# Kernel optimization log

Measured on AMD Instinct MI355X. Metric: run time of the kernel, lower is better.

## Reference

```python
import jax, jax.numpy as jnp
import numpy as np
import math

D_MODEL, N_HEADS, BATCH, SEQ = 1024, 16, 2, 2048
D_HEAD = D_MODEL // N_HEADS


def setup_inputs() -> dict:
    key = jax.random.key(0)
    ks = jax.random.split(key, 5)
    w = lambda k: jax.random.normal(k, (D_MODEL, D_MODEL), jnp.float32) * 0.02
    return {
        "X": jax.random.normal(ks[0], (BATCH, SEQ, D_MODEL), jnp.float32),
        "W_q": w(ks[1]),
        "W_k": w(ks[2]),
        "W_v": w(ks[3]),
        "W_o": w(ks[4]),
        "g_q": jnp.ones((D_MODEL,), jnp.float32),
        "b_q": jnp.zeros((D_MODEL,), jnp.float32),
        "g_k": jnp.ones((D_MODEL,), jnp.float32),
        "b_k": jnp.zeros((D_MODEL,), jnp.float32),
        "cache_k": jnp.zeros((BATCH, N_HEADS, SEQ, D_HEAD), jnp.float32),
        "cache_v": jnp.zeros((BATCH, N_HEADS, SEQ, D_HEAD), jnp.float32),
        "start_pos": 0,
    }


def _layernorm(x, g, b, eps=1e-5):
    mu = jnp.mean(x, axis=-1, keepdims=True)
    xc = x - mu
    var = jnp.mean(xc * xc, axis=-1, keepdims=True)
    return xc * jax.lax.rsqrt(var + eps) * g + b


def reference(X, W_q, W_k, W_v, W_o, g_q, b_q, g_k, b_k, cache_k, cache_v, start_pos):
    batch, N, d_model = X.shape
    H = cache_k.shape[1]
    dh = d_model // H

    # QK-normed projections (torch Linear: x @ W^T)
    XQ = _layernorm(X @ W_q.T, g_q, b_q)
    XK = _layernorm(X @ W_k.T, g_k, b_k)
    XV = X @ W_v.T
    split = lambda t: t.reshape(batch, N, H, dh).transpose(0, 2, 1, 3)  # [b,h,n,d]
    XQ, XK, XV = split(XQ), split(XK), split(XV)

    # KV-cache scatter update, then slice to valid prefix (start_pos is static)
    cache_k = jax.lax.dynamic_update_slice(cache_k, XK, (0, 0, start_pos, 0))
    cache_v = jax.lax.dynamic_update_slice(cache_v, XV, (0, 0, start_pos, 0))
    M = start_pos + N
    K = cache_k[:, :, :M]
    V = cache_v[:, :, :M]

    logits = jnp.einsum('bhnd,bhmd->bhnm', XQ, K) / math.sqrt(dh)  # [b,h,N,M]

    # causal mask on the freshly written block [start_pos:M]
    tril = jnp.tril(jnp.ones((N, N), bool))
    full_mask = jnp.concatenate([jnp.ones((N, start_pos), bool), tril], axis=1)  # [N,M]
    logits = jnp.where(full_mask[None, None], logits, -jnp.inf)

    # selective forget-mask bias built from relu'd head-0 logits
    S = jax.nn.relu(logits[:, 0])               # relu(-inf) -> 0, matches torch
    S = S.at[..., 0].set(0.0)                   # zero first column
    S = S * (1.0 - jnp.eye(N, dtype=S.dtype))   # zero diagonal (valid since start_pos==0)
    S = jnp.roll(S, 1, axis=-2)                 # shift rows down by one
    S = S.at[..., 0, :].set(0.0)
    F_mask = jnp.cumsum(S, axis=-2)             # [b,N,M]

    logits = logits - F_mask[:, None]
    attn = jax.nn.softmax(logits, axis=-1)
    O = jnp.einsum('bhnm,bhmd->bhnd', attn, V)
    O = O.transpose(0, 2, 1, 3).reshape(batch, N, d_model)
    return O @ W_o.T
```

## Files before the change

### kernel.cpp

```cpp
#include <hip/hip_runtime.h>
#include <cstdint>
#include <cstddef>


typedef unsigned short u16;
typedef __attribute__((ext_vector_type(8))) __bf16 bf16x8;
typedef __attribute__((ext_vector_type(4))) float f32x4;
typedef __attribute__((ext_vector_type(2))) unsigned int uint2v;

#define D_MODEL 1024
#define N_HEADS 16
#define BATCH   2
#define SEQ     2048
#define D_HEAD  64
#define ROWS    (BATCH*SEQ)
#define NSEG    64
#define SEGLEN  32
#define LOG2E   1.44269504f

static __device__ __forceinline__ u16 f2bf(float f){
  union { float f; uint32_t u; } v; v.f = f;
  uint32_t r = v.u + 0x7fffu + ((v.u >> 16) & 1u);
  return (u16)(r >> 16);
}
static __device__ __forceinline__ float bf2f(u16 h){
  union { uint32_t u; float f; } v; v.u = ((uint32_t)h) << 16;
  return v.f;
}
static __device__ __forceinline__ uint32_t cvtpk(float lo, float hi){
  uint32_t r;
  asm("v_cvt_pk_bf16_f32 %0, %1, %2" : "=v"(r) : "v"(lo), "v"(hi));
  return r;
}
#define GLDS(gp, lp) __builtin_amdgcn_global_load_lds( \
    (const __attribute__((address_space(1))) void*)(gp), \
    (__attribute__((address_space(3))) void*)(lp), 16, 0, 0)

__global__ void k_cast_all(const float* __restrict__ X,
                           u16* __restrict__ Xhi, u16* __restrict__ Xlo,
                           const float* __restrict__ Wq,
                           u16* __restrict__ Wqh, u16* __restrict__ Wql,
                           const float* __restrict__ Wk,
                           u16* __restrict__ Wkh, u16* __restrict__ Wkl,
                           const float* __restrict__ Wv, u16* __restrict__ Wvb,
                           const float* __restrict__ Wo, u16* __restrict__ Wob){
  int i = blockIdx.x*256 + threadIdx.x;
  if (i < 1572864){
    const float* src; u16 *dh, *dl; int base;
    if (i < 1048576){ src = X;  dh = Xhi; dl = Xlo; base = i; }
    else if (i < 1310720){ src = Wq; dh = Wqh; dl = Wql; base = i - 1048576; }
    else { src = Wk; dh = Wkh; dl = Wkl; base = i - 1310720; }
    float4 v = reinterpret_cast<const float4*>(src)[base];
    float vs[4] = {v.x, v.y, v.z, v.w};
    union { u16 s[4]; uint2 u; } uh, ul;
#pragma unroll
    for (int r=0;r<4;++r){
      uh.s[r] = f2bf(vs[r]);
      ul.s[r] = f2bf(vs[r] - bf2f(uh.s[r]));
    }
    reinterpret_cast<uint2*>(dh)[base] = uh.u;
    reinterpret_cast<uint2*>(dl)[base] = ul.u;
  } else {
    const float* src; u16* dst; int base;
    if (i < 1835008){ src = Wv; dst = Wvb; base = i - 1572864; }
    else { src = Wo; dst = Wob; base = i - 1835008; }
    float4 v = reinterpret_cast<const float4*>(src)[base];
    float vs[4] = {v.x, v.y, v.z, v.w};
    union { u16 s[4]; uint2 u; } uh;
#pragma unroll
    for (int r=0;r<4;++r) uh.s[r] = f2bf(vs[r]);
    reinterpret_cast<uint2*>(dst)[base] = uh.u;
  }
}

__global__ __launch_bounds__(256) void k_mega(
    const u16* __restrict__ Xhi, const u16* __restrict__ Xlo,
    const u16* __restrict__ Wh,  const u16* __restrict__ Wl,
    const u16* __restrict__ Wvb,
    float* __restrict__ C, float* __restrict__ Dlt, u16* __restrict__ Vt)
{
  __shared__ __align__(16) u16 smem[16384];
  const int xj = blockIdx.x & 7, q = blockIdx.x >> 3;
  int section, idx;
  if (q < 64)      { section = 0; idx = xj*64 + q; }
  else if (q < 128){ section = 1; idx = xj*64 + (q-64); }
  else             { section = 2; idx = xj*16 + (q-128); }
  const int tid = threadIdx.x, wv = tid>>6, ln = tid&63;
  const int lane15 = ln&15, quad = ln>>4;
  const int wm = wv&1, wn = wv>>1;
  const int g = ln&7, sr = ln>>3;
  const int fs = lane15 & 7;
  f32x4 z = {0.f,0.f,0.f,0.f};
  u16* As = smem;
  u16* Bs = smem + 8192;

  if (section == 2){
    const int cx = idx & 1;
    const int cy = (idx >> 1) & 31;
    const int cz = idx >> 6;
    const size_t rowBase = (size_t)cy*128;
    const size_t wbase = cx ? (size_t)1024*1024 : 0;
    const u16* Ap = cz ? Xlo : Xhi;
    const u16* Bp = (cz ? Wh : Wl) + wbase;
    f32x4 acc[4][2];
#pragma unroll
    for (int i=0;i<4;++i){ acc[i][0] = z; acc[i][1] = z; }
    for (int kt = 0; kt < 16; ++kt) {
      __syncthreads();
#pragma unroll
      for (int c = 0; c < 4; ++c) {
        int chunk = wv*4 + c, r = chunk*8 + sr;
        GLDS(Ap + (rowBase + r)*1024 + kt*64 + (g^sr)*8, As + chunk*512);
      }
#pragma unroll
      for (int c = 0; c < 2; ++c) {
        int chunk = wv*2 + c, r = chunk*8 + sr;
        GLDS(Bp + (size_t)r*1024 + kt*64 + (g^sr)*8, Bs + chunk*512);
      }
      __syncthreads();
#pragma unroll
      for (int k2=0;k2<2;++k2){
        bf16x8 af[4], bfb[2];
#pragma unroll
        for (int t=0;t<4;++t)
          af[t]  = *reinterpret_cast<const bf16x8*>(As + (wm*64 + t*16 + lane15)*64 + (((k2*4+quad)^fs)*8));
#pragma unroll
        for (int t=0;t<2;++t)
          bfb[t] = *reinterpret_cast<const bf16x8*>(Bs + (wn*32 + t*16 + lane15)*64 + (((k2*4+quad)^fs)*8));
#pragma unroll
        for (int i=0;i<4;++i)
#pragma unroll
          for (int j=0;j<2;++j)
            acc[i][j] = __builtin_amdgcn_mfma_f32_16x16x32_bf16(af[i], bfb[j], acc[i][j], 0,0,0);
      }
    }
    float* Dp = Dlt + (size_t)cz*ROWS*128;
#pragma unroll
    for (int i=0;i<4;++i){
      size_t row = rowBase + wm*64 + i*16 + quad*4;
#pragma unroll
      for (int j=0;j<2;++j){
        size_t col = (size_t)cx*64 + wn*32 + j*16 + lane15;
#pragma unroll
        for (int r=0;r<4;++r)
          Dp[(row+r)*128 + col] = acc[i][j][r];
      }
    }
  } else if (section == 0){
    const size_t rowBase = (size_t)(idx>>4)*128, colBase = (size_t)(idx&15)*128;
    f32x4 acc[4][4];
#pragma unroll
    for (int i=0;i<4;++i)
#pragma unroll
      for (int j=0;j<4;++j) acc[i][j] = z;
    for (int kt = 0; kt < 16; ++kt) {
      __syncthreads();
#pragma unroll
      for (int c = 0; c < 4; ++c) {
        int chunk = wv*4 + c, r = chunk*8 + sr;
        GLDS(Xhi + (rowBase + r)*1024 + kt*64 + (g^sr)*8, As + chunk*512);
        GLDS(Wh  + (colBase + r)*1024 + kt*64 + (g^sr)*8, Bs + chunk*512);
      }
      __syncthreads();
#pragma unroll
      for (int k2=0;k2<2;++k2){
        bf16x8 af[4], bfb[4];
#pragma unroll
        for (int t=0;t<4;++t){
          af[t]  = *reinterpret_cast<const bf16x8*>(As + (wm*64 + t*16 + lane15)*64 + (((k2*4+quad)^fs)*8));
          bfb[t] = *reinterpret_cast<const bf16x8*>(Bs + (wn*64 + t*16 + lane15)*64 + (((k2*4+quad)^fs)*8));
        }
#pragma unroll
        for (int i=0;i<4;++i)
#pragma unroll
          for (int j=0;j<4;++j)
            acc[i][j] = __builtin_amdgcn_mfma_f32_16x16x32_bf16(af[i], bfb[j], acc[i][j], 0,0,0);
      }
    }
#pragma unroll
    for (int i=0;i<4;++i){
      size_t row = rowBase + wm*64 + i*16 + quad*4;
#pragma unroll
      for (int j=0;j<4;++j){
        size_t col = colBase + wn*64 + j*16 + lane15;
#pragma unroll
        for (int r=0;r<4;++r)
          C[(row+r)*2048 + col] = acc[i][j][r];
      }
    }
  } else {
    const int bx = idx & 15, by = idx >> 4;
    const size_t rowBase = (size_t)by*128, colBase = (size_t)bx*64;
    f32x4 acc[4][2];
#pragma unroll
    for (int i=0;i<4;++i){ acc[i][0] = z; acc[i][1] = z; }
    for (int kt = 0; kt < 16; ++kt) {
      __syncthreads();
#pragma unroll
      for (int c = 0; c < 4; ++c) {
        int chunk = wv*4 + c, r = chunk*8 + sr;
        GLDS(Xhi + (rowBase + r)*1024 + kt*64 + (g^sr)*8, As + chunk*512);
      }
#pragma unroll
      for (int c = 0; c < 2; ++c) {
        int chunk = wv*2 + c, r = chunk*8 + sr;
        GLDS(Wvb + (colBase + r)*1024 + kt*64 + (g^sr)*8, Bs + chunk*512);
      }
      __syncthreads();
#pragma unroll
      for (int k2=0;k2<2;++k2){
        bf16x8 af[4], bfb[2];
#pragma unroll
        for (int t=0;t<4;++t)
          af[t]  = *reinterpret_cast<const bf16x8*>(As + (wm*64 + t*16 + lane15)*64 + (((k2*4+quad)^fs)*8));
#pragma unroll
        for (int t=0;t<2;++t)
          bfb[t] = *reinterpret_cast<const bf16x8*>(Bs + (wn*32 + t*16 + lane15)*64 + (((k2*4+quad)^fs)*8));
#pragma unroll
        for (int i=0;i<4;++i)
#pragma unroll
          for (int j=0;j<2;++j)
            acc[i][j] = __builtin_amdgcn_mfma_f32_16x16x32_bf16(af[i], bfb[j], acc[i][j], 0,0,0);
      }
    }
    __syncthreads();
#pragma unroll
    for (int i=0;i<4;++i){
      int nl = wm*64 + i*16 + quad*4;
#pragma unroll
      for (int j=0;j<2;++j){
        int dl = wn*32 + j*16 + lane15;
#pragma unroll
        for (int r=0;r<4;++r)
          smem[dl*136 + nl + r] = f2bf(acc[i][j][r]);
      }
    }
    __syncthreads();
    const int b = by >> 4;
    const int n0 = (by & 15) * 128;
    const int bh = b*N_HEADS + bx;
    const int d = tid >> 2, seg = tid & 3;
    u16* dst = Vt + ((size_t)(bh*64 + d))*SEQ + n0 + seg*32;
    const u16* srcl = smem + d*136 + seg*32;
#pragma unroll
    for (int k=0;k<4;++k)
      *reinterpret_cast<uint4*>(dst + k*8) = *reinterpret_cast<const uint4*>(srcl + k*8);
  }
}

__global__ __launch_bounds__(256) void k_ln_pack2(
    const float* __restrict__ C, const float* __restrict__ Dlt,
    const float* __restrict__ gq, const float* __restrict__ bq,
    const float* __restrict__ gk, const float* __restrict__ bk,
    u16* __restrict__ Qh, u16* __restrict__ Kh,
    u16* __restrict__ Q0l, u16* __restrict__ K0l)
{
  const int row = blockIdx.x;
  const int tid = threadIdx.x;
  const float* cr = C + (size_t)row*2048;
  float4 vq = reinterpret_cast<const float4*>(cr)[tid];
  float4 vk = reinterpret_cast<const float4*>(cr)[256 + tid];
  const int h = tid >> 4;
  if (h == 0){
    const float* D0 = Dlt + (size_t)row*128;
    const float* D1 = Dlt + (size_t)ROWS*128 + (size_t)row*128;
    float4 a0 = reinterpret_cast<const float4*>(D0)[tid&15];
    float4 a1 = reinterpret_cast<const float4*>(D1)[tid&15];
    vq.x+=a0.x+a1.x; vq.y+=a0.y+a1.y; vq.z+=a0.z+a1.z; vq.w+=a0.w+a1.w;
    float4 b0 = reinterpret_cast<const float4*>(D0 + 64)[tid&15];
    float4 b1 = reinterpret_cast<const float4*>(D1 + 64)[tid&15];
    vk.x+=b0.x+b1.x; vk.y+=b0.y+b1.y; vk.z+=b0.z+b1.z; vk.w+=b0.w+b1.w;
  }
  float sq  = vq.x+vq.y+vq.z+vq.w;
  float s2q = vq.x*vq.x+vq.y*vq.y+vq.z*vq.z+vq.w*vq.w;
  float sk  = vk.x+vk.y+vk.z+vk.w;
  float s2k = vk.x*vk.x+vk.y*vk.y+vk.z*vk.z+vk.w*vk.w;
#pragma unroll
  for (int o=32;o;o>>=1){
    sq += __shfl_xor(sq,o);  s2q += __shfl_xor(s2q,o);
    sk += __shfl_xor(sk,o);  s2k += __shfl_xor(s2k,o);
  }
  __shared__ float red[4][4];
  if ((tid&63)==0){
    red[tid>>6][0]=sq; red[tid>>6][1]=s2q; red[tid>>6][2]=sk; red[tid>>6][3]=s2k;
  }
  __syncthreads();
  sq  = red[0][0]+red[1][0]+red[2][0]+red[3][0];
  s2q = red[0][1]+red[1][1]+red[2][1]+red[3][1];
  sk  = red[0][2]+red[1][2]+red[2][2]+red[3][2];
  s2k = red[0][3]+red[1][3]+red[2][3]+red[3][3];
  const float muq = sq*(1.f/D_MODEL);
  const float rsq = rsqrtf(s2q*(1.f/D_MODEL) - muq*muq + 1e-5f);
  const float muk = sk*(1.f/D_MODEL);
  const float rsk = rsqrtf(s2k*(1.f/D_MODEL) - muk*muk + 1e-5f);
  const int b = row >> 11, n = row & (SEQ-1);
  const int d0 = (tid & 15)*4;
  float4 gqv = reinterpret_cast<const float4*>(gq)[tid];
  float4 bqv = reinterpret_cast<const float4*>(bq)[tid];
  float4 gkv = reinterpret_cast<const float4*>(gk)[tid];
  float4 bkv = reinterpret_cast<const float4*>(bk)[tid];
  float xq[4] = {vq.x,vq.y,vq.z,vq.w}, xk[4] = {vk.x,vk.y,vk.z,vk.w};
  float gQ[4] = {gqv.x,gqv.y,gqv.z,gqv.w}, bQ[4] = {bqv.x,bqv.y,bqv.z,bqv.w};
  float gK[4] = {gkv.x,gkv.y,gkv.z,gkv.w}, bK[4] = {bkv.x,bkv.y,bkv.z,bkv.w};
  union { u16 s[4]; uint2 u; } qh, ql, kh, kl;
#pragma unroll
  for (int r=0;r<4;++r){
    float yq = (xq[r]-muq)*rsq*gQ[r] + bQ[r];
    qh.s[r] = f2bf(yq);
    ql.s[r] = f2bf(yq - bf2f(qh.s[r]));
    float yk = (xk[r]-muk)*rsk*gK[r] + bK[r];
    kh.s[r] = f2bf(yk);
    kl.s[r] = f2bf(yk - bf2f(kh.s[r]));
  }
  size_t dst = (((size_t)(b*N_HEADS + h))*SEQ + n)*D_HEAD + d0;
  *reinterpret_cast<uint2*>(Qh + dst) = qh.u;
  *reinterpret_cast<uint2*>(Kh + dst) = kh.u;
  if (h == 0){
    size_t dl = ((size_t)b*SEQ + n)*D_HEAD + d0;
    *reinterpret_cast<uint2*>(Q0l + dl) = ql.u;
    *reinterpret_cast<uint2*>(K0l + dl) = kl.u;
  }
}

__global__ __launch_bounds__(256) void k_s0(
    const u16* Qh, const u16* Q0l, const u16* Kh, const u16* K0l,
    float* __restrict__ S0, float* __restrict__ seg)
{
  const int b = blockIdx.z;
  const int bm = blockIdx.y;
  const int bn = blockIdx.x;
  const int tid = threadIdx.x;
  if (bn > bm){
    for (int t = tid; t < 512; t += 256)
      seg[((size_t)b*NSEG + bm*4 + (t>>7))*SEQ + bn*128 + (t&127)] = 0.f;
    return;
  }
  float* Sb = S0 + (size_t)b*SEQ*SEQ;
  __shared__ __align__(16) u16 smem[4*8192];
  const int wv = tid>>6, ln = tid&63;
  const int lane15 = ln&15, quad = ln>>4;
  const int wm = wv&1, wn = wv>>1;
  const int g = ln&7, sr = ln>>3;
  const int fs = lane15 & 7;
  const size_t rowBase = (size_t)bm*128, colBase = (size_t)bn*128;
  const u16* srcs[4] = {
    Qh  + ((size_t)b*N_HEADS*SEQ + rowBase)*D_HEAD,
    Q0l + ((size_t)b*SEQ + rowBase)*D_HEAD,
    Kh  + ((size_t)b*N_HEADS*SEQ + colBase)*D_HEAD,
    K0l + ((size_t)b*SEQ + colBase)*D_HEAD };
#pragma unroll
  for (int t=0;t<4;++t){
#pragma unroll
    for (int c=0;c<4;++c){
      int chunk = wv*4 + c, r = chunk*8 + sr;
      GLDS(srcs[t] + (size_t)r*64 + (g^sr)*8, smem + t*8192 + chunk*512);
    }
  }
  __syncthreads();
  f32x4 acc[4][4];
  f32x4 z = {0.f,0.f,0.f,0.f};
#pragma unroll
  for (int i=0;i<4;++i)
#pragma unroll
    for (int j=0;j<4;++j) acc[i][j] = z;
  const int Aidx[3] = {0, 0, 1};
  const int Bidx[3] = {2, 3, 2};
#pragma unroll
  for (int p = 0; p < 3; ++p){
    const u16* At = smem + Aidx[p]*8192;
    const u16* Bt = smem + Bidx[p]*8192;
#pragma unroll
    for (int k2=0;k2<2;++k2){
      bf16x8 af[4], bfb[4];
#pragma unroll
      for (int t=0;t<4;++t){
        af[t]  = *reinterpret_cast<const bf16x8*>(At + (wm*64 + t*16 + lane15)*64 + (((k2*4+quad)^fs)*8));
        bfb[t] = *reinterpret_cast<const bf16x8*>(Bt + (wn*64 + t*16 + lane15)*64 + (((k2*4+quad)^fs)*8));
      }
#pragma unroll
      for (int i=0;i<4;++i)
#pragma unroll
        for (int j=0;j<4;++j)
          acc[i][j] = __builtin_amdgcn_mfma_f32_16x16x32_bf16(af[i], bfb[j], acc[i][j], 0,0,0);
    }
  }
  float csum[2][4] = {{0.f,0.f,0.f,0.f},{0.f,0.f,0.f,0.f}};
#pragma unroll
  for (int i=0;i<4;++i){
#pragma unroll
    for (int j=0;j<4;++j){
#pragma unroll
      for (int r=0;r<4;++r){
        int jg = (int)rowBase + wm*64 + i*16 + quad*4 + r;
        int mg = (int)colBase + wn*64 + j*16 + lane15;
        float l = acc[i][j][r]*0.125f;
        float s = (mg >= 1 && mg < jg) ? fmaxf(l, 0.f) : 0.f;
        Sb[(size_t)jg*SEQ + mg] = s;
        csum[i>>1][j] += s;
      }
    }
  }
  __syncthreads();
  float* cs = (float*)smem;
#pragma unroll
  for (int h2=0;h2<2;++h2){
#pragma unroll
    for (int j=0;j<4;++j){
      float v = csum[h2][j];
      v += __shfl_xor(v, 16);
      v += __shfl_xor(v, 32);
      if (ln < 16) cs[(wm*2 + h2)*128 + wn*64 + j*16 + ln] = v;
    }
  }
  __syncthreads();
  for (int t = tid; t < 512; t += 256)
    seg[((size_t)b*NSEG + bm*4 + (t>>7))*SEQ + bn*128 + (t&127)] = cs[t];
}

__global__ void k_seg_apply(float* __restrict__ SF, const float* __restrict__ seg){
  int m = blockIdx.x*256 + threadIdx.x;
  int s = blockIdx.y, b = blockIdx.z;
  const float* sb = seg + (size_t)b*NSEG*SEQ;
  float run = 0.f;
  for (int t=0; t<s; ++t) run += sb[(size_t)t*SEQ + m];
  float* Sb = SF + (size_t)b*SEQ*SEQ;
  const int j0 = s*SEGLEN;
#pragma unroll 8
  for (int i=0;i<SEGLEN;++i){
    size_t idx = (size_t)(j0 + i)*SEQ + m;
    float t = Sb[idx];
    Sb[idx] = -run*LOG2E;
    run += (j0 + i > m) ? t : 0.f;
  }
}

__constant__ unsigned char WMAP[48] = {
  62,63,60,79,
  61,58,59,56,78,
  57,54,55,52,77,
  53,50,51,48,76,
  49,46,47,44,75,
  45,42,43,40,74,
  41,38,39,36,73,
  37,34,35,32,72,
  33,71,
  70,69,68,67,66,65,64};

__global__ __launch_bounds__(256, 4) void k_attn(
    const u16* __restrict__ Qh, const u16* __restrict__ Kh,
    const u16* __restrict__ Vt, const float* __restrict__ F,
    u16* __restrict__ Ob, float* __restrict__ Opart, float* __restrict__ Ps)
{
  __shared__ __align__(16) u16 Ks[2][64*64];
  __shared__ __align__(16) u16 Vs[2][64*64];
  const int w = blockIdx.x;
  const int bh = w & 31, b = bh >> 4, h = bh & 15;
  const int item = (int)WMAP[w >> 5];
  int nt, mt0, mt1, segi;
  if (item >= 64){ nt = item - 64; segi = 0; mt0 = 0; mt1 = nt; }
  else {
    nt = item >> 1; segi = item & 1;
    const int half = (nt + 2) >> 1;
    mt0 = segi ? half : 0;
    mt1 = segi ? nt : (half - 1);
  }
  const bool partial = (item < 64);
  const int tid = threadIdx.x, wv = tid>>6, ln = tid&63;
  const int lane15 = ln&15, quad = ln>>4;
  const u16* Qbh = Qh + ((size_t)(b*N_HEADS + h))*SEQ*D_HEAD;
  const u16* Kbh = Kh + ((size_t)(b*N_HEADS + h))*SEQ*D_HEAD;
  const u16* Vbh = Vt + ((size_t)(b*N_HEADS + h))*D_HEAD*SEQ;
  const int n_loc = wv*16 + lane15;
  const int n_g = nt*64 + n_loc;
  const float* Frow = F + (size_t)b*SEQ*SEQ + (size_t)n_g*SEQ;
  const int swz = (ln&7) ^ ((ln>>3)&7);
  const int fswz = lane15 & 7;
  const int srow = ln>>3;

  bf16x8 qf[2];
#pragma unroll
  for (int kt=0; kt<2; ++kt)
    qf[kt] = *reinterpret_cast<const bf16x8*>(Qbh + (size_t)n_g*D_HEAD + kt*32 + quad*8);

  f32x4 z = {0.f,0.f,0.f,0.f};
  f32x4 psum = z;
  f32x4 acc_o[4];
#pragma unroll
  for (int no=0;no<4;++no) acc_o[no] = z;

  auto stage = [&](int mt, int buf){
#pragma unroll
    for (int c=0;c<2;++c){
      int chunk = wv*2 + c;
      int r = chunk*8 + srow;
      GLDS(Kbh + (size_t)(mt*64 + r)*D_HEAD + swz*8, &Ks[buf][chunk*512]);
      GLDS(Vbh + (size_t)r*SEQ + mt*64 + swz*8,      &Vs[buf][chunk*512]);
    }
  };
  stage(mt0, mt0 & 1);
  f32x4 fvn[4];
#pragma unroll
  for (int ms=0; ms<4; ++ms)
    fvn[ms] = *reinterpret_cast<const f32x4*>(Frow + mt0*64 + ms*16 + quad*4);
  const float c1 = 0.125f*LOG2E;

  for (int mt = mt0; mt <= mt1; ++mt) {
    const int cur = mt & 1;
    __syncthreads();
    if (mt < mt1) stage(mt+1, 1-cur);
    f32x4 fv[4];
#pragma unroll
    for (int ms=0; ms<4; ++ms) fv[ms] = fvn[ms];
    if (mt < mt1){
      const float* Fr1 = Frow + (mt+1)*64;
#pragma unroll
      for (int ms=0; ms<4; ++ms)
        fvn[ms] = *reinterpret_cast<const f32x4*>(Fr1 + ms*16 + quad*4);
    }
    f32x4 accs[4];
    __builtin_amdgcn_s_setprio(1);
#pragma unroll
    for (int ms=0; ms<4; ++ms){
      bf16x8 a = *reinterpret_cast<const bf16x8*>(
          &Ks[cur][(ms*16 + lane15)*64 + ((quad ^ fswz) * 8)]);
      accs[ms] = __builtin_amdgcn_mfma_f32_16x16x32_bf16(a, qf[0], z, 0,0,0);
    }
#pragma unroll
    for (int ms=0; ms<4; ++ms){
      bf16x8 a = *reinterpret_cast<const bf16x8*>(
          &Ks[cur][(ms*16 + lane15)*64 + (((4 + quad) ^ fswz) * 8)]);
      accs[ms] = __builtin_amdgcn_mfma_f32_16x16x32_bf16(a, qf[1], accs[ms], 0,0,0);
    }
    __builtin_amdgcn_s_setprio(0);
    uint32_t pw[4][2];
    if (mt == nt){
#pragma unroll
      for (int ms=0; ms<4; ++ms){
        const int ml = ms*16 + quad*4;
        float l0 = fmaf(accs[ms][0], c1, fv[ms][0]);
        float l1 = fmaf(accs[ms][1], c1, fv[ms][1]);
        float l2 = fmaf(accs[ms][2], c1, fv[ms][2]);
        float l3 = fmaf(accs[ms][3], c1, fv[ms][3]);
        if (ml + 0 > n_loc) l0 = -1e30f;
        if (ml + 1 > n_loc) l1 = -1e30f;
        if (ml + 2 > n_loc) l2 = -1e30f;
        if (ml + 3 > n_loc) l3 = -1e30f;
        float p0 = __builtin_amdgcn_exp2f(l0);
        float p1 = __builtin_amdgcn_exp2f(l1);
        float p2 = __builtin_amdgcn_exp2f(l2);
        float p3 = __builtin_amdgcn_exp2f(l3);
        psum[0]+=p0; psum[1]+=p1; psum[2]+=p2; psum[3]+=p3;
        pw[ms][0] = cvtpk(p0, p1);
        pw[ms][1] = cvtpk(p2, p3);
      }
    } else {
#pragma unroll
      for (int ms=0; ms<4; ++ms){
        float p0 = __builtin_amdgcn_exp2f(fmaf(accs[ms][0], c1, fv[ms][0]));
        float p1 = __builtin_amdgcn_exp2f(fmaf(accs[ms][1], c1, fv[ms][1]));
        float p2 = __builtin_amdgcn_exp2f(fmaf(accs[ms][2], c1, fv[ms][2]));
        float p3 = __builtin_amdgcn_exp2f(fmaf(accs[ms][3], c1, fv[ms][3]));
        psum[0]+=p0; psum[1]+=p1; psum[2]+=p2; psum[3]+=p3;
        pw[ms][0] = cvtpk(p0, p1);
        pw[ms][1] = cvtpk(p2, p3);
      }
    }
    __builtin_amdgcn_s_setprio(1);
#pragma unroll
    for (int kt=0; kt<2; ++kt){
      union { uint32_t u[4]; bf16x8 v; } pa;
#pragma unroll
      for (int pr=0; pr<2; ++pr){
        uint2v s32 = __builtin_amdgcn_permlane32_swap(
            pw[2*kt][pr], pw[2*kt+1][pr], false, false);
        uint2v s16 = __builtin_amdgcn_permlane16_swap(s32.x, s32.y, false, false);
        pa.u[pr]   = s16.x;
        pa.u[2+pr] = s16.y;
      }
#pragma unroll
      for (int no=0; no<4; ++no){
        int d = no*16 + lane15;
        bf16x8 vb = *reinterpret_cast<const bf16x8*>(
            &Vs[cur][d*64 + (((kt*4 + quad) ^ (d&7)) * 8)]);
        acc_o[no] = __builtin_amdgcn_mfma_f32_16x16x32_bf16(pa.v, vb, acc_o[no], 0,0,0);
      }
    }
    __builtin_amdgcn_s_setprio(0);
  }
  float s = (psum[0]+psum[1]) + (psum[2]+psum[3]);
  s += __shfl_xor(s, 16);
  s += __shfl_xor(s, 32);
  if (partial){
    const size_t pb = (size_t)(bh*16 + (nt - 16))*2 + segi;
    float* Op = Opart + pb*4096;
    if (quad == 0) Ps[pb*64 + wv*16 + lane15] = s;
#pragma unroll
    for (int no=0; no<4; ++no)
#pragma unroll
      for (int r=0;r<4;++r)
        Op[(wv*16 + quad*4 + r)*64 + no*16 + lane15] = acc_o[no][r];
  } else {
    f32x4 inv;
#pragma unroll
    for (int r=0;r<4;++r)
      inv[r] = __builtin_amdgcn_rcpf(__shfl(s, quad*4 + r));
#pragma unroll
    for (int no=0; no<4; ++no){
#pragma unroll
      for (int r=0;r<4;++r){
        float o = acc_o[no][r] * inv[r];
        int row = nt*64 + wv*16 + quad*4 + r;
        Ob[((size_t)(b*SEQ + row))*D_MODEL + h*64 + no*16 + lane15] = f2bf(o);
      }
    }
  }
}

__global__ __launch_bounds__(256) void k_comb(
    const float* __restrict__ Opart, const float* __restrict__ Ps,
    u16* __restrict__ Ob)
{
  const int t = blockIdx.x;
  const int bh = t >> 4, b = bh >> 4, h = bh & 15;
  const int nt = (t & 15) + 16;
  const int tid = threadIdx.x;
  const int row = tid >> 2, c0 = (tid & 3) * 16;
  const float* P0 = Opart + (size_t)t*2*4096 + row*64 + c0;
  const float* P1 = P0 + 4096;
  const float s = Ps[(size_t)t*128 + row] + Ps[(size_t)t*128 + 64 + row];
  const float inv = __builtin_amdgcn_rcpf(s);
  union { u16 us[16]; uint4 u[2]; } o;
#pragma unroll
  for (int g2=0; g2<4; ++g2){
    float4 a = reinterpret_cast<const float4*>(P0)[g2];
    float4 c = reinterpret_cast<const float4*>(P1)[g2];
    o.us[g2*4+0] = f2bf((a.x + c.x) * inv);
    o.us[g2*4+1] = f2bf((a.y + c.y) * inv);
    o.us[g2*4+2] = f2bf((a.z + c.z) * inv);
    o.us[g2*4+3] = f2bf((a.w + c.w) * inv);
  }
  u16* dst = Ob + ((size_t)(b*SEQ + nt*64 + row))*D_MODEL + h*64 + c0;
  reinterpret_cast<uint4*>(dst)[0] = o.u[0];
  reinterpret_cast<uint4*>(dst)[1] = o.u[1];
}

__global__ __launch_bounds__(256) void k_gemm_nt64(
    const u16* __restrict__ A0, const u16* __restrict__ B0,
    float* __restrict__ C, int N, int K)
{
  __shared__ __align__(16) u16 As[8192];
  __shared__ __align__(16) u16 Bs[4096];
  const int tid = threadIdx.x, wv = tid>>6, ln = tid&63;
  const int lane15 = ln&15, quad = ln>>4;
  const int wm = wv&1, wn = wv>>1;
  const int g = ln&7, sr = ln>>3;
  const int fs = lane15 & 7;
  const size_t rowBase = (size_t)blockIdx.y*128, colBase = (size_t)blockIdx.x*64;
  f32x4 acc[4][2];
  f32x4 z = {0.f,0.f,0.f,0.f};
#pragma unroll
  for (int i=0;i<4;++i){ acc[i][0] = z; acc[i][1] = z; }
  const int ktiles = K >> 6;
  for (int kt = 0; kt < ktiles; ++kt) {
    __syncthreads();
#pragma unroll
    for (int c = 0; c < 4; ++c) {
      int chunk = wv*4 + c, r = chunk*8 + sr;
      GLDS(A0 + (rowBase + r)*K + kt*64 + (g^sr)*8, As + chunk*512);
    }
#pragma unroll
    for (int c = 0; c < 2; ++c) {
      int chunk = wv*2 + c, r = chunk*8 + sr;
      GLDS(B0 + (colBase + r)*K + kt*64 + (g^sr)*8, Bs + chunk*512);
    }
    __syncthreads();
#pragma unroll
    for (int k2=0;k2<2;++k2){
      bf16x8 af[4], bfb[2];
#pragma unroll
      for (int t=0;t<4;++t)
        af[t]  = *reinterpret_cast<const bf16x8*>(As + (wm*64 + t*16 + lane15)*64 + (((k2*4+quad)^fs)*8));
#pragma unroll
      for (int t=0;t<2;++t)
        bfb[t] = *reinterpret_cast<const bf16x8*>(Bs + (wn*32 + t*16 + lane15)*64 + (((k2*4+quad)^fs)*8));
#pragma unroll
      for (int i=0;i<4;++i)
#pragma unroll
        for (int j=0;j<2;++j)
          acc[i][j] = __builtin_amdgcn_mfma_f32_16x16x32_bf16(af[i], bfb[j], acc[i][j], 0,0,0);
    }
  }
#pragma unroll
  for (int i=0;i<4;++i){
    size_t row = rowBase + wm*64 + i*16 + quad*4;
#pragma unroll
    for (int j=0;j<2;++j){
      size_t col = colBase + wn*32 + j*16 + lane15;
#pragma unroll
      for (int r=0;r<4;++r)
        C[(row+r)*N + col] = acc[i][j][r];
    }
  }
}

extern "C" void kernel_launch(void* const* d_in, const int* in_sizes, int n_in,
                              void* d_out, int out_size, void* d_ws, size_t ws_size,
                              hipStream_t stream)
{
  (void)in_sizes; (void)n_in; (void)out_size; (void)ws_size;
  const float* X  = (const float*)d_in[0];
  const float* Wq = (const float*)d_in[1];
  const float* Wk = (const float*)d_in[2];
  const float* Wv = (const float*)d_in[3];
  const float* Wo = (const float*)d_in[4];
  const float* gq = (const float*)d_in[5];
  const float* bq = (const float*)d_in[6];
  const float* gk = (const float*)d_in[7];
  const float* bk = (const float*)d_in[8];
  float* out = (float*)d_out;

  char* ws = (char*)d_ws;
  size_t off = 0;
  auto alloc = [&](size_t bytes)->char*{
    char* p = ws + off; off += (bytes + 255) & ~(size_t)255; return p;
  };
  u16* Xhi  = (u16*)alloc((size_t)ROWS*D_MODEL*2);
  u16* Xlo  = (u16*)alloc((size_t)ROWS*D_MODEL*2);
  u16* Wqkh = (u16*)alloc((size_t)2*D_MODEL*D_MODEL*2);
  u16* Wqkl = (u16*)alloc((size_t)2*D_MODEL*D_MODEL*2);
  u16* Wvb  = (u16*)alloc((size_t)D_MODEL*D_MODEL*2);
  u16* Wob  = (u16*)alloc((size_t)D_MODEL*D_MODEL*2);
  u16* Qhp  = (u16*)alloc((size_t)BATCH*N_HEADS*SEQ*D_HEAD*2);
  u16* Khp  = (u16*)alloc((size_t)BATCH*N_HEADS*SEQ*D_HEAD*2);
  u16* Q0l  = (u16*)alloc((size_t)BATCH*SEQ*D_HEAD*2);
  u16* K0l  = (u16*)alloc((size_t)BATCH*SEQ*D_HEAD*2);
  u16* Vtp  = (u16*)alloc((size_t)BATCH*N_HEADS*D_HEAD*SEQ*2);
  u16* Obf  = (u16*)alloc((size_t)ROWS*D_MODEL*2);
  float* Dlt = (float*)alloc((size_t)2*ROWS*128*4);
  float* Seg = (float*)alloc((size_t)BATCH*NSEG*SEQ*4);
  float* Opart = (float*)alloc((size_t)512*2*4096*4);
  float* Ps    = (float*)alloc((size_t)512*2*64*4);
  float* SF  = (float*)alloc((size_t)BATCH*SEQ*SEQ*4);
  float* C32 = SF;

  k_cast_all<<<8192, 256, 0, stream>>>(
      X, Xhi, Xlo,
      Wq, Wqkh, Wqkl,
      Wk, Wqkh + (size_t)D_MODEL*D_MODEL, Wqkl + (size_t)D_MODEL*D_MODEL,
      Wv, Wvb, Wo, Wob);
  k_mega<<<1152, 256, 0, stream>>>(Xhi, Xlo, Wqkh, Wqkl, Wvb, C32, Dlt, Vtp);
  k_ln_pack2<<<ROWS, 256, 0, stream>>>(C32, Dlt, gq, bq, gk, bk, Qhp, Khp, Q0l, K0l);
  k_s0<<<dim3(16, 16, BATCH), 256, 0, stream>>>(Qhp, Q0l, Khp, K0l, SF, Seg);
  k_seg_apply<<<dim3(8, NSEG, BATCH), 256, 0, stream>>>(SF, Seg);
  k_attn<<<1536, 256, 0, stream>>>(Qhp, Khp, Vtp, SF, Obf, Opart, Ps);
  k_comb<<<512, 256, 0, stream>>>(Opart, Ps, Obf);
  k_gemm_nt64<<<dim3(16, 32), 256, 0, stream>>>(Obf, Wob, out, D_MODEL, D_MODEL);
}
```

Before: 283.5 us.

## Triple-buffer K/V tiles in attention kernel with two-ahead prefetch

Grows the shared K/V staging from two buffers to three and restructures the main loop so tile mt+2 is loaded while mt is computed. A manual vmcnt wait plus a raw barrier replaces __syncthreads in the steady state, with a tail loop for the last two tiles. The aim is to hide global-to-LDS latency more deeply, at the cost of more LDS per block (48KB), which may reduce occupancy under launch_bounds(256,4). The vmcnt(8) count depends on exact instruction counts, including the F loads, which makes it fragile.

Result: no change. 288.2 us (+1.7%).

```diff
diff --git a/kernel.cpp b/kernel.cpp
--- a/kernel.cpp
+++ b/kernel.cpp
@@ -451,8 +451,8 @@
     const u16* __restrict__ Vt, const float* __restrict__ F,
     u16* __restrict__ Ob, float* __restrict__ Opart, float* __restrict__ Ps)
 {
-  __shared__ __align__(16) u16 Ks[2][64*64];
-  __shared__ __align__(16) u16 Vs[2][64*64];
+  __shared__ __align__(16) u16 Ks[3][64*64];
+  __shared__ __align__(16) u16 Vs[3][64*64];
   const int w = blockIdx.x;
   const int bh = w & 31, b = bh >> 4, h = bh & 15;
   const int item = (int)WMAP[w >> 5];
@@ -497,38 +497,22 @@
       GLDS(Vbh + (size_t)r*SEQ + mt*64 + swz*8,      &Vs[buf][chunk*512]);
     }
   };
-  stage(mt0, mt0 & 1);
-  f32x4 fvn[4];
-#pragma unroll
-  for (int ms=0; ms<4; ++ms)
-    fvn[ms] = *reinterpret_cast<const f32x4*>(Frow + mt0*64 + ms*16 + quad*4);
   const float c1 = 0.125f*LOG2E;
-
-  for (int mt = mt0; mt <= mt1; ++mt) {
-    const int cur = mt & 1;
-    __syncthreads();
-    if (mt < mt1) stage(mt+1, 1-cur);
-    f32x4 fv[4];
-#pragma unroll
-    for (int ms=0; ms<4; ++ms) fv[ms] = fvn[ms];
-    if (mt < mt1){
-      const float* Fr1 = Frow + (mt+1)*64;
-#pragma unroll
-      for (int ms=0; ms<4; ++ms)
-        fvn[ms] = *reinterpret_cast<const f32x4*>(Fr1 + ms*16 + quad*4);
-    }
+  f32x4 fv[4], fvn[4];
+
+  auto compute = [&](int mt, int bi){
     f32x4 accs[4];
     __builtin_amdgcn_s_setprio(1);
 #pragma unroll
     for (int ms=0; ms<4; ++ms){
       bf16x8 a = *reinterpret_cast<const bf16x8*>(
-          &Ks[cur][(ms*16 + lane15)*64 + ((quad ^ fswz) * 8)]);
+          &Ks[bi][(ms*16 + lane15)*64 + ((quad ^ fswz) * 8)]);
       accs[ms] = __builtin_amdgcn_mfma_f32_16x16x32_bf16(a, qf[0], z, 0,0,0);
     }
 #pragma unroll
     for (int ms=0; ms<4; ++ms){
       bf16x8 a = *reinterpret_cast<const bf16x8*>(
-          &Ks[cur][(ms*16 + lane15)*64 + (((4 + quad) ^ fswz) * 8)]);
+          &Ks[bi][(ms*16 + lane15)*64 + (((4 + quad) ^ fswz) * 8)]);
       accs[ms] = __builtin_amdgcn_mfma_f32_16x16x32_bf16(a, qf[1], accs[ms], 0,0,0);
     }
     __builtin_amdgcn_s_setprio(0);
@@ -581,12 +565,47 @@
       for (int no=0; no<4; ++no){
         int d = no*16 + lane15;
         bf16x8 vb = *reinterpret_cast<const bf16x8*>(
-            &Vs[cur][d*64 + (((kt*4 + quad) ^ (d&7)) * 8)]);
+            &Vs[bi][d*64 + (((kt*4 + quad) ^ (d&7)) * 8)]);
         acc_o[no] = __builtin_amdgcn_mfma_f32_16x16x32_bf16(pa.v, vb, acc_o[no], 0,0,0);
       }
     }
     __builtin_amdgcn_s_setprio(0);
-  }
+  };
+
+  stage(mt0, 0);
+#pragma unroll
+  for (int ms=0; ms<4; ++ms)
+    fvn[ms] = *reinterpret_cast<const f32x4*>(Frow + mt0*64 + ms*16 + quad*4);
+  if (mt0 < mt1) stage(mt0+1, 1);
+
+  int mt = mt0;
+  for (; mt <= mt1 - 2; ++mt){
+    asm volatile("s_waitcnt vmcnt(8)" ::: "memory");
+    __builtin_amdgcn_sched_barrier(0);
+    __builtin_amdgcn_s_barrier();
+    __builtin_amdgcn_sched_barrier(0);
+#pragma unroll
+    for (int ms=0; ms<4; ++ms) fv[ms] = fvn[ms];
+    const float* Fr1 = Frow + (mt+1)*64;
+#pragma unroll
+    for (int ms=0; ms<4; ++ms)
+      fvn[ms] = *reinterpret_cast<const f32x4*>(Fr1 + ms*16 + quad*4);
+    stage(mt+2, (mt+2-mt0) % 3);
+    compute(mt, (mt-mt0) % 3);
+  }
+  for (; mt <= mt1; ++mt){
+    __syncthreads();
+#pragma unroll
+    for (int ms=0; ms<4; ++ms) fv[ms] = fvn[ms];
+    if (mt < mt1){
+      const float* Fr1 = Frow + (mt+1)*64;
+#pragma unroll
+      for (int ms=0; ms<4; ++ms)
+        fvn[ms] = *reinterpret_cast<const f32x4*>(Fr1 + ms*16 + quad*4);
+    }
+    compute(mt, (mt-mt0) % 3);
+  }
+
   float s = (psum[0]+psum[1]) + (psum[2]+psum[3]);
   s += __shfl_xor(s, 16);
   s += __shfl_xor(s, 32);
```
